# Performance work log

Hardware: AMD Instinct MI355X
Metric: run time of the kernel (lower is better)

The kernel has to match this reference:

```python
import jax, jax.numpy as jnp
import numpy as np

N = 50000      # nodes
E = 800000     # edges (before self-loops)
F_IN = 128
F_OUT = 128
H = 4          # heads
SLOPE = 0.2    # LeakyReLU negative slope (PyG GATConv default)


def setup_inputs() -> dict:
    key = jax.random.key(0)
    ks = jax.random.split(key, 8)
    x = jax.random.normal(ks[0], (N, F_IN), dtype=jnp.float32)
    edge_index = jax.random.randint(ks[1], (2, E), 0, N, dtype=jnp.int64)
    W = jax.random.normal(ks[2], (H, F_IN, F_OUT), dtype=jnp.float32) * (1.0 / np.sqrt(F_IN))
    att_src = jax.random.normal(ks[3], (H, F_OUT), dtype=jnp.float32) * (1.0 / np.sqrt(F_OUT))
    att_dst = jax.random.normal(ks[4], (H, F_OUT), dtype=jnp.float32) * (1.0 / np.sqrt(F_OUT))
    bias = jnp.zeros((H, F_OUT), dtype=jnp.float32)
    W_out = jax.random.normal(ks[5], (H * F_OUT, F_OUT), dtype=jnp.float32) * (1.0 / np.sqrt(H * F_OUT))
    b_out = jnp.zeros((F_OUT,), dtype=jnp.float32)
    return {"x": x, "edge_index": edge_index, "W": W, "att_src": att_src,
            "att_dst": att_dst, "bias": bias, "W_out": W_out, "b_out": b_out}


def _gat_head(x, src, dst, W_h, a_src, a_dst, b_h):
    # x: [N, F_in]; src/dst: [E'] edge endpoints (messages flow src -> dst)
    xW = x @ W_h                                   # [N, F_out]
    alpha_s = xW @ a_src                           # [N]
    alpha_d = xW @ a_dst                           # [N]
    logits = alpha_s[src] + alpha_d[dst]           # [E']
    logits = jnp.where(logits > 0, logits, SLOPE * logits)  # leaky_relu
    # segment softmax over edges grouped by destination node
    seg_max = jax.ops.segment_max(logits, dst, num_segments=N)  # [N]
    e = jnp.exp(logits - seg_max[dst])             # [E']
    denom = jax.ops.segment_sum(e, dst, num_segments=N)         # [N]
    alpha = e / denom[dst]                         # [E']
    # weighted scatter-aggregate of source features to destinations
    out = jax.ops.segment_sum(alpha[:, None] * xW[src], dst, num_segments=N)  # [N, F_out]
    return out + b_h


def reference(x, edge_index, W, att_src, att_dst, bias, W_out, b_out):
    # add self-loops (PyG GATConv default)
    loops = jnp.arange(N, dtype=edge_index.dtype)
    src = jnp.concatenate([edge_index[0], loops])
    dst = jnp.concatenate([edge_index[1], loops])
    heads = [_gat_head(x, src, dst, W[h], att_src[h], att_dst[h], bias[h]) for h in range(H)]
    h_cat = jnp.concatenate(heads, axis=1)         # [N, H*F_out]
    return jax.nn.relu(h_cat @ W_out + b_out)      # [N, F_out]
```

## Files before the change

### kernel.cpp

```cpp
#include <hip/hip_runtime.h>
#include <hip/hip_bf16.h>

constexpr int NN = 50000;
constexpr int EE = 800000;
constexpr float SLOPE = 0.2f;
constexpr int CAP = 64;
constexpr int ZE = NN * CAP;
constexpr int LDP = 520;

typedef __bf16 bf16x8 __attribute__((ext_vector_type(8)));
typedef __bf16 bf16x4 __attribute__((ext_vector_type(4)));
typedef float f32x4 __attribute__((ext_vector_type(4)));
typedef float f32x2 __attribute__((ext_vector_type(2)));

__device__ __forceinline__ int edge_at(const int* e32, const long long* e64, int use64, long i) {
    return use64 ? (int)e64[i] : e32[i];
}

__device__ __forceinline__ f32x2 bfpair(unsigned u) {
    f32x2 r;
    r.x = __uint_as_float(u << 16);
    r.y = __uint_as_float(u & 0xffff0000u);
    return r;
}

__global__ void k_prec(const float* __restrict__ W, const float* __restrict__ Wout,
                       const float* __restrict__ att_s, const float* __restrict__ att_d,
                       const float* __restrict__ bias, const float* __restrict__ bout,
                       const long long* e64, int* flag, int* cnt,
                       __bf16* __restrict__ Bfrag, float* __restrict__ wsv, float* __restrict__ wdv,
                       float* __restrict__ cvec, uint4* __restrict__ ew) {
    int b = blockIdx.x, t = threadIdx.x;
    if (b < 512) {
        int h = b >> 7, k = b & 127;
        float acc = 0.f;
        for (int j = 0; j < 128; j++) {
            float w = W[((size_t)(h * 128 + k)) * 128 + j];
            acc += w * Wout[((size_t)(h * 128 + j)) * 128 + t];
        }
        int K = h * 128 + k;
        int k0i = K >> 5, kb = (K >> 3) & 3, jj = K & 7;
        int ni = t >> 4, lr = t & 15;
        Bfrag[(((size_t)k0i * 8 + ni) * 64 + kb * 16 + lr) * 8 + jj] = (__bf16)acc;
    } else if (b == 512) {
        float acc = bout[t];
        for (int j = 0; j < 512; j++) acc += bias[j] * Wout[(size_t)j * 128 + t];
        cvec[t] = acc;
        if (t == 0) ew[ZE] = make_uint4(0u, 0u, 0u, 0u);
    } else if (b < 517) {
        int h = b - 513;
        float as = 0.f, ad = 0.f;
        for (int j = 0; j < 128; j++) {
            float w = W[((size_t)(h * 128 + t)) * 128 + j];
            as += w * att_s[h * 128 + j];
            ad += w * att_d[h * 128 + j];
        }
        wsv[h * 128 + t] = as;
        wdv[h * 128 + t] = ad;
    } else {
        int i = (b - 517) * 128 + t;
        if (i < NN) cnt[i] = 0;
        if (b == 517 && t < 64) {
            long long v = e64[t];
            bool ok = (v >= 0) && (v < (long long)NN);
            unsigned long long m = __ballot(ok);
            if (t == 0) *flag = (m == 0xFFFFFFFFFFFFFFFFull) ? 1 : 0;
        }
    }
}

__global__ __launch_bounds__(256) void k_prep(const float* __restrict__ x, const float* __restrict__ wsv,
                                              const float* __restrict__ wdv, __bf16* __restrict__ xb,
                                              float* __restrict__ as_, float* __restrict__ ad_) {
    int n = blockIdx.x * blockDim.x + threadIdx.x;
    if (n >= NN) return;
    const float4* xr = (const float4*)(x + (size_t)n * 128);
    __bf16* xo = xb + (size_t)n * 128;
    float s[4] = {0, 0, 0, 0}, d[4] = {0, 0, 0, 0};
    for (int q = 0; q < 32; q += 2) {
        float4 v0 = xr[q], v1 = xr[q + 1];
        bf16x8 o;
        o[0] = (__bf16)v0.x; o[1] = (__bf16)v0.y; o[2] = (__bf16)v0.z; o[3] = (__bf16)v0.w;
        o[4] = (__bf16)v1.x; o[5] = (__bf16)v1.y; o[6] = (__bf16)v1.z; o[7] = (__bf16)v1.w;
        *(bf16x8*)(xo + q * 4) = o;
        #pragma unroll
        for (int h = 0; h < 4; h++) {
            float4 a0 = ((const float4*)(wsv + h * 128))[q];
            float4 a1 = ((const float4*)(wsv + h * 128))[q + 1];
            float4 b0 = ((const float4*)(wdv + h * 128))[q];
            float4 b1 = ((const float4*)(wdv + h * 128))[q + 1];
            s[h] += v0.x * a0.x + v0.y * a0.y + v0.z * a0.z + v0.w * a0.w
                  + v1.x * a1.x + v1.y * a1.y + v1.z * a1.z + v1.w * a1.w;
            d[h] += v0.x * b0.x + v0.y * b0.y + v0.z * b0.z + v0.w * b0.w
                  + v1.x * b1.x + v1.y * b1.y + v1.z * b1.z + v1.w * b1.w;
        }
    }
    #pragma unroll
    for (int h = 0; h < 4; h++) { as_[n * 4 + h] = s[h]; ad_[n * 4 + h] = d[h]; }
}

__global__ __launch_bounds__(256) void k_scatterB(const int* e32, const long long* e64, const int* flag,
                                                  const float* __restrict__ as_, const float* __restrict__ ad_,
                                                  int* cnt, uint4* __restrict__ ew) {
    long i0 = ((long)blockIdx.x * blockDim.x + threadIdx.x) * 2;
    if (i0 >= (long)EE + NN) return;
    int use64 = *flag;
    int s[2], d[2];
    #pragma unroll
    for (int j = 0; j < 2; j++) {
        long i = i0 + j;
        if (i < EE) { s[j] = edge_at(e32, e64, use64, i); d[j] = edge_at(e32, e64, use64, (long)EE + i); }
        else        { s[j] = (int)(i - EE); d[j] = s[j]; }
    }
    float4 av[2], bv[2];
    #pragma unroll
    for (int j = 0; j < 2; j++) av[j] = *(const float4*)(as_ + (size_t)s[j] * 4);
    #pragma unroll
    for (int j = 0; j < 2; j++) bv[j] = *(const float4*)(ad_ + (size_t)d[j] * 4);
    int pos[2];
    #pragma unroll
    for (int j = 0; j < 2; j++) pos[j] = d[j] * CAP + atomicAdd(&cnt[d[j]], 1);
    #pragma unroll
    for (int j = 0; j < 2; j++) {
        float l0 = av[j].x + bv[j].x; l0 = l0 > 0.f ? l0 : SLOPE * l0;
        float l1 = av[j].y + bv[j].y; l1 = l1 > 0.f ? l1 : SLOPE * l1;
        float l2 = av[j].z + bv[j].z; l2 = l2 > 0.f ? l2 : SLOPE * l2;
        float l3 = av[j].w + bv[j].w; l3 = l3 > 0.f ? l3 : SLOPE * l3;
        bf16x4 w;
        w[0] = (__bf16)__expf(l0);
        w[1] = (__bf16)__expf(l1);
        w[2] = (__bf16)__expf(l2);
        w[3] = (__bf16)__expf(l3);
        uint2 wp = *(uint2*)&w;
        ew[pos[j]] = make_uint4((unsigned)s[j], wp.x, wp.y, 0u);
    }
}

__global__ __launch_bounds__(256) void k_aggF(const int* __restrict__ cnt, const uint4* __restrict__ ew,
                                              const __bf16* __restrict__ xb, const __bf16* __restrict__ Bfrag,
                                              const float* __restrict__ cvec, float* __restrict__ y) {
    __shared__ __bf16 aggL[16 * LDP];
    int t = threadIdx.x;
    int lane = t & 63;
    int half = lane >> 5;
    int sub = lane & 31;
    int hw = ((t >> 6) << 1) + half;
    size_t fo = 4 * (size_t)sub;

    #pragma unroll
    for (int r = 0; r < 2; r++) {
        int nl = r * 8 + hw;
        int n = blockIdx.x * 16 + nl;
        int deg = cnt[n];
        int beg = n * CAP;
        int last = beg + deg - 1;
        int dmax = max(deg, __shfl_xor(deg, 32));
        int nit = (dmax + 3) >> 2;
        f32x2 a01[4] = {}, a23[4] = {};
        f32x2 dn01 = {0.f, 0.f}, dn23 = {0.f, 0.f};
        int e = beg;
        for (int it = 0; it < nit; ++it, e += 4) {
            int i0 = (e     <= last) ? e     : ZE;
            int i1 = (e + 1 <= last) ? e + 1 : ZE;
            int i2 = (e + 2 <= last) ? e + 2 : ZE;
            int i3 = (e + 3 <= last) ? e + 3 : ZE;
            uint4 r0 = ew[i0], r1 = ew[i1], r2 = ew[i2], r3 = ew[i3];
            uint2 x0 = *(const uint2*)(xb + (size_t)r0.x * 128 + fo);
            uint2 x1 = *(const uint2*)(xb + (size_t)r1.x * 128 + fo);
            uint2 x2 = *(const uint2*)(xb + (size_t)r2.x * 128 + fo);
            uint2 x3 = *(const uint2*)(xb + (size_t)r3.x * 128 + fo);
#define ACCP(R, XR) { \
            f32x2 w01 = bfpair(R.y), w23 = bfpair(R.z); \
            f32x2 x01 = bfpair(XR.x), x23 = bfpair(XR.y); \
            f32x2 q0 = {w01.x, w01.x}, q1 = {w01.y, w01.y}; \
            f32x2 q2 = {w23.x, w23.x}, q3 = {w23.y, w23.y}; \
            a01[0] += q0 * x01; a23[0] += q0 * x23; \
            a01[1] += q1 * x01; a23[1] += q1 * x23; \
            a01[2] += q2 * x01; a23[2] += q2 * x23; \
            a01[3] += q3 * x01; a23[3] += q3 * x23; \
            dn01 += w01; dn23 += w23; }
            ACCP(r0, x0) ACCP(r1, x1) ACCP(r2, x2) ACCP(r3, x3)
#undef ACCP
        }
        float inv[4];
        inv[0] = 1.f / dn01.x; inv[1] = 1.f / dn01.y;
        inv[2] = 1.f / dn23.x; inv[3] = 1.f / dn23.y;
        __bf16* ar = aggL + nl * LDP + fo;
        #pragma unroll
        for (int h = 0; h < 4; h++) {
            bf16x4 o;
            o[0] = (__bf16)(a01[h].x * inv[h]); o[1] = (__bf16)(a01[h].y * inv[h]);
            o[2] = (__bf16)(a23[h].x * inv[h]); o[3] = (__bf16)(a23[h].y * inv[h]);
            *(bf16x4*)(ar + h * 128) = o;
        }
    }
    __syncthreads();

    int w = t >> 6;
    int lr = lane & 15, kb = lane >> 4;
    f32x4 acc[2] = {};
    for (int k0i = 0; k0i < 16; k0i++) {
        bf16x8 a = *(const bf16x8*)(aggL + lr * LDP + k0i * 32 + kb * 8);
        #pragma unroll
        for (int ni = 0; ni < 2; ni++) {
            int ni_g = w * 2 + ni;
            bf16x8 b = *(const bf16x8*)(Bfrag + (((size_t)k0i * 8 + ni_g) * 64 + lane) * 8);
            acc[ni] = __builtin_amdgcn_mfma_f32_16x16x32_bf16(a, b, acc[ni], 0, 0, 0);
        }
    }
    int row0 = blockIdx.x * 16 + kb * 4;
    #pragma unroll
    for (int ni = 0; ni < 2; ni++) {
        int c = (w * 2 + ni) * 16 + lr;
        float cv = cvec[c];
        #pragma unroll
        for (int r = 0; r < 4; r++) {
            y[(size_t)(row0 + r) * 128 + c] = fmaxf(acc[ni][r] + cv, 0.f);
        }
    }
}

extern "C" void kernel_launch(void* const* d_in, const int* in_sizes, int n_in,
                              void* d_out, int out_size, void* d_ws, size_t ws_size,
                              hipStream_t stream) {
    const float* x     = (const float*)d_in[0];
    const void*  ei    = d_in[1];
    const float* W     = (const float*)d_in[2];
    const float* att_s = (const float*)d_in[3];
    const float* att_d = (const float*)d_in[4];
    const float* bias  = (const float*)d_in[5];
    const float* Wout  = (const float*)d_in[6];
    const float* bout  = (const float*)d_in[7];
    float* y = (float*)d_out;

    const int* e32 = (const int*)ei;
    const long long* e64 = (const long long*)ei;

    char* ws = (char*)d_ws;
    size_t off = 0;
    auto alloc = [&](size_t bytes) -> void* {
        void* p = ws + off;
        off = (off + bytes + 255) & ~(size_t)255;
        return p;
    };
    __bf16* xb    = (__bf16*)alloc((size_t)NN * 128 * 2);
    uint4* ew     = (uint4*)alloc(((size_t)NN * CAP + 1) * 16);
    float* as_    = (float*)alloc((size_t)NN * 4 * 4);
    float* ad_    = (float*)alloc((size_t)NN * 4 * 4);
    __bf16* Bfrag = (__bf16*)alloc((size_t)512 * 128 * 2);
    float* wsv    = (float*)alloc(4 * 128 * 4);
    float* wdv    = (float*)alloc(4 * 128 * 4);
    float* cvec   = (float*)alloc(128 * 4);
    int* cnt      = (int*)alloc((size_t)NN * 4);
    int* flag     = (int*)alloc(4);

    int precBlocks = 517 + (NN + 127) / 128;
    k_prec<<<precBlocks, 128, 0, stream>>>(W, Wout, att_s, att_d, bias, bout,
                                           e64, flag, cnt, Bfrag, wsv, wdv, cvec, ew);
    k_prep<<<(NN + 255) / 256, 256, 0, stream>>>(x, wsv, wdv, xb, as_, ad_);
    k_scatterB<<<((EE + NN) / 2 + 255) / 256, 256, 0, stream>>>(e32, e64, flag, as_, ad_, cnt, ew);
    k_aggF<<<NN / 16, 256, 0, stream>>>(cnt, ew, xb, Bfrag, cvec, y);
}
```

Measured before the change: 135.6 us.

## Sort nodes by degree for balanced aggregation and software-pipeline edge record loads

Adds histogram, scan and permutation kernels that order destination nodes by in-degree, so each aggregation block processes nodes with similar degree and the two half-waves sharing a loop bound waste fewer iterations. The aggregation loop also prefetches the next group of four edge records while processing the current one, to hide gather latency. Output rows are scattered through the permutation via a shared node-id table. This costs three extra small launches, heavy contention on a handful of histogram atomics, and non-contiguous output row writes.

Measured after the change: 417.3 us. 3.08x slower.

```diff
diff --git a/kernel.cpp b/kernel.cpp
--- a/kernel.cpp
+++ b/kernel.cpp
@@ -27,7 +27,7 @@
 __global__ void k_prec(const float* __restrict__ W, const float* __restrict__ Wout,
                        const float* __restrict__ att_s, const float* __restrict__ att_d,
                        const float* __restrict__ bias, const float* __restrict__ bout,
-                       const long long* e64, int* flag, int* cnt,
+                       const long long* e64, int* flag, int* cnt, int* dhist,
                        __bf16* __restrict__ Bfrag, float* __restrict__ wsv, float* __restrict__ wdv,
                        float* __restrict__ cvec, uint4* __restrict__ ew) {
     int b = blockIdx.x, t = threadIdx.x;
@@ -46,6 +46,7 @@
         float acc = bout[t];
         for (int j = 0; j < 512; j++) acc += bias[j] * Wout[(size_t)j * 128 + t];
         cvec[t] = acc;
+        if (t <= 64 + 1) dhist[t] = 0;
         if (t == 0) ew[ZE] = make_uint4(0u, 0u, 0u, 0u);
     } else if (b < 517) {
         int h = b - 513;
@@ -136,10 +137,39 @@
     }
 }
 
-__global__ __launch_bounds__(256) void k_aggF(const int* __restrict__ cnt, const uint4* __restrict__ ew,
+__global__ void k_dhist(const int* __restrict__ cnt, int* __restrict__ dhist) {
+    int n = blockIdx.x * blockDim.x + threadIdx.x;
+    if (n < NN) atomicAdd(&dhist[cnt[n]], 1);
+}
+
+__global__ void k_dscan(int* dhist) {
+    __shared__ int l[128];
+    int t = threadIdx.x;
+    int orig = (t < 65) ? dhist[t] : 0;
+    l[t] = orig;
+    __syncthreads();
+    for (int o = 1; o < 128; o <<= 1) {
+        int v = (t >= o) ? l[t - o] : 0;
+        __syncthreads();
+        l[t] += v;
+        __syncthreads();
+    }
+    if (t < 65) dhist[t] = l[t] - orig;
+}
+
+__global__ void k_dperm(const int* __restrict__ cnt, int* __restrict__ dhist, int* __restrict__ perm) {
+    int n = blockIdx.x * blockDim.x + threadIdx.x;
+    if (n >= NN) return;
+    int p = atomicAdd(&dhist[cnt[n]], 1);
+    perm[p] = n;
+}
+
+__global__ __launch_bounds__(256) void k_aggF(const int* __restrict__ cnt, const int* __restrict__ perm,
+                                              const uint4* __restrict__ ew,
                                               const __bf16* __restrict__ xb, const __bf16* __restrict__ Bfrag,
                                               const float* __restrict__ cvec, float* __restrict__ y) {
     __shared__ __bf16 aggL[16 * LDP];
+    __shared__ int nid[16];
     int t = threadIdx.x;
     int lane = t & 63;
     int half = lane >> 5;
@@ -150,7 +180,8 @@
     #pragma unroll
     for (int r = 0; r < 2; r++) {
         int nl = r * 8 + hw;
-        int n = blockIdx.x * 16 + nl;
+        int n = perm[blockIdx.x * 16 + nl];
+        if (sub == 0) nid[nl] = n;
         int deg = cnt[n];
         int beg = n * CAP;
         int last = beg + deg - 1;
@@ -159,12 +190,18 @@
         f32x2 a01[4] = {}, a23[4] = {};
         f32x2 dn01 = {0.f, 0.f}, dn23 = {0.f, 0.f};
         int e = beg;
-        for (int it = 0; it < nit; ++it, e += 4) {
-            int i0 = (e     <= last) ? e     : ZE;
-            int i1 = (e + 1 <= last) ? e + 1 : ZE;
-            int i2 = (e + 2 <= last) ? e + 2 : ZE;
-            int i3 = (e + 3 <= last) ? e + 3 : ZE;
-            uint4 r0 = ew[i0], r1 = ew[i1], r2 = ew[i2], r3 = ew[i3];
+        int i0 = (e     <= last) ? e     : ZE;
+        int i1 = (e + 1 <= last) ? e + 1 : ZE;
+        int i2 = (e + 2 <= last) ? e + 2 : ZE;
+        int i3 = (e + 3 <= last) ? e + 3 : ZE;
+        uint4 r0 = ew[i0], r1 = ew[i1], r2 = ew[i2], r3 = ew[i3];
+        for (int it = 0; it < nit; ++it) {
+            e += 4;
+            int p0 = (e     <= last) ? e     : ZE;
+            int p1 = (e + 1 <= last) ? e + 1 : ZE;
+            int p2 = (e + 2 <= last) ? e + 2 : ZE;
+            int p3 = (e + 3 <= last) ? e + 3 : ZE;
+            uint4 n0 = ew[p0], n1 = ew[p1], n2 = ew[p2], n3 = ew[p3];
             uint2 x0 = *(const uint2*)(xb + (size_t)r0.x * 128 + fo);
             uint2 x1 = *(const uint2*)(xb + (size_t)r1.x * 128 + fo);
             uint2 x2 = *(const uint2*)(xb + (size_t)r2.x * 128 + fo);
@@ -181,6 +218,7 @@
             dn01 += w01; dn23 += w23; }
             ACCP(r0, x0) ACCP(r1, x1) ACCP(r2, x2) ACCP(r3, x3)
 #undef ACCP
+            r0 = n0; r1 = n1; r2 = n2; r3 = n3;
         }
         float inv[4];
         inv[0] = 1.f / dn01.x; inv[1] = 1.f / dn01.y;
@@ -208,14 +246,14 @@
             acc[ni] = __builtin_amdgcn_mfma_f32_16x16x32_bf16(a, b, acc[ni], 0, 0, 0);
         }
     }
-    int row0 = blockIdx.x * 16 + kb * 4;
     #pragma unroll
     for (int ni = 0; ni < 2; ni++) {
         int c = (w * 2 + ni) * 16 + lr;
         float cv = cvec[c];
         #pragma unroll
         for (int r = 0; r < 4; r++) {
-            y[(size_t)(row0 + r) * 128 + c] = fmaxf(acc[ni][r] + cv, 0.f);
+            int row = kb * 4 + r;
+            y[(size_t)nid[row] * 128 + c] = fmaxf(acc[ni][r] + cv, 0.f);
         }
     }
 }
@@ -252,12 +290,17 @@
     float* wdv    = (float*)alloc(4 * 128 * 4);
     float* cvec   = (float*)alloc(128 * 4);
     int* cnt      = (int*)alloc((size_t)NN * 4);
+    int* perm     = (int*)alloc((size_t)NN * 4);
+    int* dhist    = (int*)alloc(128 * 4);
     int* flag     = (int*)alloc(4);
 
     int precBlocks = 517 + (NN + 127) / 128;
     k_prec<<<precBlocks, 128, 0, stream>>>(W, Wout, att_s, att_d, bias, bout,
-                                           e64, flag, cnt, Bfrag, wsv, wdv, cvec, ew);
+                                           e64, flag, cnt, dhist, Bfrag, wsv, wdv, cvec, ew);
     k_prep<<<(NN + 255) / 256, 256, 0, stream>>>(x, wsv, wdv, xb, as_, ad_);
     k_scatterB<<<((EE + NN) / 2 + 255) / 256, 256, 0, stream>>>(e32, e64, flag, as_, ad_, cnt, ew);
-    k_aggF<<<NN / 16, 256, 0, stream>>>(cnt, ew, xb, Bfrag, cvec, y);
-}
+    k_dhist<<<(NN + 255) / 256, 256, 0, stream>>>(cnt, dhist);
+    k_dscan<<<1, 128, 0, stream>>>(dhist);
+    k_dperm<<<(NN + 255) / 256, 256, 0, stream>>>(cnt, dhist, perm);
+    k_aggF<<<NN / 16, 256, 0, stream>>>(cnt, perm, ew, xb, Bfrag, cvec, y);
+}
```

## Prefetch next edge records in aggregation, shrink bucket capacity, one edge per scatter thread

Applied to the files above, without the earlier changes.

The aggregation loop now loads the next group of four packed edge records while it processes the current group, so the index fetch latency overlaps the feature gathers and FMAs. The per-node bucket capacity drops from 64 to 48, which shrinks the edge buffer and its memory footprint. The scatter kernel goes back to one edge per thread with a grid twice as large. Risks: the prefetch adds register pressure and one redundant load group per node, and CAP=48 overflows if any node's in-degree plus self-loop exceeds 48. With random edges the mean in-degree is about 17, so that is unlikely but not guaranteed.

Result: slower. 139.3 us (+2.8%).

```diff
diff --git a/kernel.cpp b/kernel.cpp
--- a/kernel.cpp
+++ b/kernel.cpp
@@ -4,7 +4,7 @@
 constexpr int NN = 50000;
 constexpr int EE = 800000;
 constexpr float SLOPE = 0.2f;
-constexpr int CAP = 64;
+constexpr int CAP = 48;
 constexpr int ZE = NN * CAP;
 constexpr int LDP = 520;
 
@@ -102,38 +102,26 @@
 __global__ __launch_bounds__(256) void k_scatterB(const int* e32, const long long* e64, const int* flag,
                                                   const float* __restrict__ as_, const float* __restrict__ ad_,
                                                   int* cnt, uint4* __restrict__ ew) {
-    long i0 = ((long)blockIdx.x * blockDim.x + threadIdx.x) * 2;
-    if (i0 >= (long)EE + NN) return;
+    long i = (long)blockIdx.x * blockDim.x + threadIdx.x;
+    if (i >= (long)EE + NN) return;
     int use64 = *flag;
-    int s[2], d[2];
-    #pragma unroll
-    for (int j = 0; j < 2; j++) {
-        long i = i0 + j;
-        if (i < EE) { s[j] = edge_at(e32, e64, use64, i); d[j] = edge_at(e32, e64, use64, (long)EE + i); }
-        else        { s[j] = (int)(i - EE); d[j] = s[j]; }
-    }
-    float4 av[2], bv[2];
-    #pragma unroll
-    for (int j = 0; j < 2; j++) av[j] = *(const float4*)(as_ + (size_t)s[j] * 4);
-    #pragma unroll
-    for (int j = 0; j < 2; j++) bv[j] = *(const float4*)(ad_ + (size_t)d[j] * 4);
-    int pos[2];
-    #pragma unroll
-    for (int j = 0; j < 2; j++) pos[j] = d[j] * CAP + atomicAdd(&cnt[d[j]], 1);
-    #pragma unroll
-    for (int j = 0; j < 2; j++) {
-        float l0 = av[j].x + bv[j].x; l0 = l0 > 0.f ? l0 : SLOPE * l0;
-        float l1 = av[j].y + bv[j].y; l1 = l1 > 0.f ? l1 : SLOPE * l1;
-        float l2 = av[j].z + bv[j].z; l2 = l2 > 0.f ? l2 : SLOPE * l2;
-        float l3 = av[j].w + bv[j].w; l3 = l3 > 0.f ? l3 : SLOPE * l3;
-        bf16x4 w;
-        w[0] = (__bf16)__expf(l0);
-        w[1] = (__bf16)__expf(l1);
-        w[2] = (__bf16)__expf(l2);
-        w[3] = (__bf16)__expf(l3);
-        uint2 wp = *(uint2*)&w;
-        ew[pos[j]] = make_uint4((unsigned)s[j], wp.x, wp.y, 0u);
-    }
+    int s, d;
+    if (i < EE) { s = edge_at(e32, e64, use64, i); d = edge_at(e32, e64, use64, (long)EE + i); }
+    else        { s = (int)(i - EE); d = s; }
+    float4 av = *(const float4*)(as_ + (size_t)s * 4);
+    float4 bv = *(const float4*)(ad_ + (size_t)d * 4);
+    float l0 = av.x + bv.x; l0 = l0 > 0.f ? l0 : SLOPE * l0;
+    float l1 = av.y + bv.y; l1 = l1 > 0.f ? l1 : SLOPE * l1;
+    float l2 = av.z + bv.z; l2 = l2 > 0.f ? l2 : SLOPE * l2;
+    float l3 = av.w + bv.w; l3 = l3 > 0.f ? l3 : SLOPE * l3;
+    bf16x4 w;
+    w[0] = (__bf16)__expf(l0);
+    w[1] = (__bf16)__expf(l1);
+    w[2] = (__bf16)__expf(l2);
+    w[3] = (__bf16)__expf(l3);
+    uint2 wp = *(uint2*)&w;
+    int pos = d * CAP + atomicAdd(&cnt[d], 1);
+    ew[pos] = make_uint4((unsigned)s, wp.x, wp.y, 0u);
 }
 
 __global__ __launch_bounds__(256) void k_aggF(const int* __restrict__ cnt, const uint4* __restrict__ ew,
@@ -159,12 +147,18 @@
         f32x2 a01[4] = {}, a23[4] = {};
         f32x2 dn01 = {0.f, 0.f}, dn23 = {0.f, 0.f};
         int e = beg;
-        for (int it = 0; it < nit; ++it, e += 4) {
-            int i0 = (e     <= last) ? e     : ZE;
-            int i1 = (e + 1 <= last) ? e + 1 : ZE;
-            int i2 = (e + 2 <= last) ? e + 2 : ZE;
-            int i3 = (e + 3 <= last) ? e + 3 : ZE;
-            uint4 r0 = ew[i0], r1 = ew[i1], r2 = ew[i2], r3 = ew[i3];
+        int i0 = (e     <= last) ? e     : ZE;
+        int i1 = (e + 1 <= last) ? e + 1 : ZE;
+        int i2 = (e + 2 <= last) ? e + 2 : ZE;
+        int i3 = (e + 3 <= last) ? e + 3 : ZE;
+        uint4 r0 = ew[i0], r1 = ew[i1], r2 = ew[i2], r3 = ew[i3];
+        for (int it = 0; it < nit; ++it) {
+            e += 4;
+            int p0 = (e     <= last) ? e     : ZE;
+            int p1 = (e + 1 <= last) ? e + 1 : ZE;
+            int p2 = (e + 2 <= last) ? e + 2 : ZE;
+            int p3 = (e + 3 <= last) ? e + 3 : ZE;
+            uint4 n0 = ew[p0], n1 = ew[p1], n2 = ew[p2], n3 = ew[p3];
             uint2 x0 = *(const uint2*)(xb + (size_t)r0.x * 128 + fo);
             uint2 x1 = *(const uint2*)(xb + (size_t)r1.x * 128 + fo);
             uint2 x2 = *(const uint2*)(xb + (size_t)r2.x * 128 + fo);
@@ -181,6 +175,7 @@
             dn01 += w01; dn23 += w23; }
             ACCP(r0, x0) ACCP(r1, x1) ACCP(r2, x2) ACCP(r3, x3)
 #undef ACCP
+            r0 = n0; r1 = n1; r2 = n2; r3 = n3;
         }
         float inv[4];
         inv[0] = 1.f / dn01.x; inv[1] = 1.f / dn01.y;
@@ -258,6 +253,6 @@
     k_prec<<<precBlocks, 128, 0, stream>>>(W, Wout, att_s, att_d, bias, bout,
                                            e64, flag, cnt, Bfrag, wsv, wdv, cvec, ew);
     k_prep<<<(NN + 255) / 256, 256, 0, stream>>>(x, wsv, wdv, xb, as_, ad_);
-    k_scatterB<<<((EE + NN) / 2 + 255) / 256, 256, 0, stream>>>(e32, e64, flag, as_, ad_, cnt, ew);
+    k_scatterB<<<(EE + NN + 255) / 256, 256, 0, stream>>>(e32, e64, flag, as_, ad_, cnt, ew);
     k_aggF<<<NN / 16, 256, 0, stream>>>(cnt, ew, xb, Bfrag, cvec, y);
 }
```
